# Performance work log

Measured on AMD Instinct MI355X. Metric: run time of the kernel, lower is better.

The kernel has to match this reference:

```python
import jax, jax.numpy as jnp
import numpy as np

B, T, D = 2, 2048, 1024
NH, DH = 16, 64  # inner = NH*DH = D
SCALE_INIT = 0.02


def setup_inputs() -> dict:
    key = jax.random.key(0)
    kx, kq, kk, kv, ko = jax.random.split(key, 5)
    return {
        "x": jax.random.normal(kx, (B, T, D), dtype=jnp.float32),
        "Wq": jax.random.normal(kq, (D, NH * DH), dtype=jnp.float32) * SCALE_INIT,
        "Wk": jax.random.normal(kk, (D, NH * DH), dtype=jnp.float32) * SCALE_INIT,
        "Wv": jax.random.normal(kv, (D, NH * DH), dtype=jnp.float32) * SCALE_INIT,
        "Wo": jax.random.normal(ko, (NH * DH, D), dtype=jnp.float32) * SCALE_INIT,
    }


def reference(x, Wq, Wk, Wv, Wo):
    # x: (B, T, D)
    b, t, _ = x.shape

    def split_heads(h):
        # (B, T, NH*DH) -> (B, NH, T, DH)
        return h.reshape(b, t, NH, DH).transpose(0, 2, 1, 3)

    q = split_heads(x @ Wq)
    k = split_heads(x @ Wk)
    v = split_heads(x @ Wv)

    scale = jnp.asarray(1.0 / np.sqrt(DH), dtype=x.dtype)
    # The per-chunk loop in the original is mathematically equivalent to
    # full causal attention: each query row attends to keys with k_pos <= q_pos.
    scores = jnp.einsum("bhqd,bhkd->bhqk", q, k) * scale  # (B, NH, T, T)
    causal_mask = jnp.arange(t)[None, :] > jnp.arange(t)[:, None]  # k_pos > q_pos
    scores = jnp.where(causal_mask, -jnp.inf, scores)
    attn = jax.nn.softmax(scores, axis=-1)
    attn = jnp.nan_to_num(attn)  # matches torch.nan_to_num (no fully-masked rows in causal case)
    o = jnp.einsum("bhqk,bhkd->bhqd", attn, v)  # (B, NH, T, DH)
    o = o.transpose(0, 2, 1, 3).reshape(b, t, NH * DH)  # merge heads
    return o @ Wo  # (B, T, D)
```

## Files before the change

### kernel.cpp

```cpp
#include <hip/hip_runtime.h>
#include <hip/hip_bf16.h>
#include <string.h>

#define Bsz 2
#define Tsz 2048
#define Dsz 1024
#define NHsz 16
#define Msz (Bsz*Tsz)

typedef unsigned short bfu;
typedef __attribute__((ext_vector_type(8))) short short8;
typedef __attribute__((ext_vector_type(4))) short short4v;
typedef __attribute__((ext_vector_type(4))) float floatx4;

__device__ __forceinline__ bfu f2bf(float f) {
  unsigned int u = __builtin_bit_cast(unsigned int, f);
  u += 0x7fffu + ((u >> 16) & 1u);
  return (bfu)(u >> 16);
}

__device__ __forceinline__ short4v pack4bf(float a, float b, float c_, float d) {
  __hip_bfloat162 h01 = __float22bfloat162_rn(make_float2(a, b));
  __hip_bfloat162 h23 = __float22bfloat162_rn(make_float2(c_, d));
  uint2 uu;
  memcpy(&uu.x, &h01, 4);
  memcpy(&uu.y, &h23, 4);
  return __builtin_bit_cast(short4v, uu);
}

__device__ __forceinline__ short8 pack8bf(float4 a, float4 b) {
  __hip_bfloat162 h0 = __float22bfloat162_rn(make_float2(a.x, a.y));
  __hip_bfloat162 h1 = __float22bfloat162_rn(make_float2(a.z, a.w));
  __hip_bfloat162 h2 = __float22bfloat162_rn(make_float2(b.x, b.y));
  __hip_bfloat162 h3 = __float22bfloat162_rn(make_float2(b.z, b.w));
  uint4 u;
  memcpy(&u.x, &h0, 4); memcpy(&u.y, &h1, 4);
  memcpy(&u.z, &h2, 4); memcpy(&u.w, &h3, 4);
  return __builtin_bit_cast(short8, u);
}

__device__ __forceinline__ void async16(const void* g, void* l) {
  void* gnc = (void*)g;
  __builtin_amdgcn_global_load_lds((__attribute__((address_space(1))) void*)gnc,
                                   (__attribute__((address_space(3))) void*)l,
                                   16, 0, 0);
}

__global__ __launch_bounds__(256) void transpose_w(const float* __restrict__ W0, const float* __restrict__ W1,
                                                   const float* __restrict__ W2, const float* __restrict__ W3,
                                                   bfu* __restrict__ wt) {
  __shared__ float tile[32][33];
  const float* W = blockIdx.z == 0 ? W0 : blockIdx.z == 1 ? W1 : blockIdx.z == 2 ? W2 : W3;
  const float s = (blockIdx.z == 0) ? 0.18033688011112042f : 1.0f;
  bfu* WT = wt + (size_t)blockIdx.z * Dsz * Dsz;
  int tx = threadIdx.x, ty = threadIdx.y;
  int kb = blockIdx.y * 32, nb = blockIdx.x * 32;
#pragma unroll
  for (int i = 0; i < 4; ++i)
    tile[ty + i*8][tx] = W[(size_t)(kb + ty + i*8) * Dsz + nb + tx];
  __syncthreads();
#pragma unroll
  for (int i = 0; i < 4; ++i)
    WT[(size_t)(nb + ty + i*8) * Dsz + kb + tx] = f2bf(tile[tx][ty + i*8] * s);
}

template <bool F32OUT, bool AF32, int NT>
__global__ __launch_bounds__(256) void gemm128(const void* __restrict__ Ain, const bfu* __restrict__ Bt0,
                                               void* __restrict__ C0, int K, int N,
                                               size_t strideB, size_t strideC) {
  constexpr int NJ = NT / 32;
  const int tid = threadIdx.x, wave = tid >> 6, lane = tid & 63;
  const int g = lane >> 4, c = lane & 15;
  const int m0 = blockIdx.y * 128, n0 = blockIdx.x * NT;
  const bfu* Bt = Bt0 + strideB * blockIdx.z;
  __shared__ bfu smem[4096 + NT * 32];
  bfu* As = smem;
  bfu* Bs = smem + 4096;
  floatx4 acc[4][NJ] = {};
  const int srow = lane >> 2, scol = (lane & 3) * 8;
  const bfu* gB = Bt + (size_t)(n0 + srow) * K + scol;
  const int wm = (wave >> 1) * 64, wn = (wave & 1) * (NT / 2);

  short8 areg[2];
  if (AF32) {
#pragma unroll
    for (int cc = 0; cc < 2; ++cc) {
      const float* pa = (const float*)Ain +
          (size_t)(m0 + (wave*2 + cc)*16 + srow) * K + scol;
      areg[cc] = pack8bf(((const float4*)pa)[0], ((const float4*)pa)[1]);
    }
  }
  const bfu* gA = AF32 ? nullptr : (const bfu*)Ain + (size_t)(m0 + srow) * K + scol;

  for (int k0 = 0; k0 < K; k0 += 32) {
    __syncthreads();
#pragma unroll
    for (int cc = 0; cc < 2; ++cc) {
      const int chunk = wave * 2 + cc;
      if (AF32) *(short8*)&As[chunk * 512 + lane * 8] = areg[cc];
      else      async16(gA + (size_t)chunk * 16 * K + k0, &As[chunk * 512]);
    }
#pragma unroll
    for (int cc = 0; cc < NT/64; ++cc) {
      const int chunk = wave * (NT/64) + cc;
      async16(gB + (size_t)chunk * 16 * K + k0, &Bs[chunk * 512]);
    }
    __syncthreads();
    if (AF32 && k0 + 32 < K) {
#pragma unroll
      for (int cc = 0; cc < 2; ++cc) {
        const float* pa = (const float*)Ain +
            (size_t)(m0 + (wave*2 + cc)*16 + srow) * K + (k0 + 32) + scol;
        areg[cc] = pack8bf(((const float4*)pa)[0], ((const float4*)pa)[1]);
      }
    }
    short8 afr[4], bfr[NJ];
#pragma unroll
    for (int t = 0; t < 4; ++t) afr[t] = *(const short8*)&As[(wm + t*16 + c) * 32 + g * 8];
#pragma unroll
    for (int t = 0; t < NJ; ++t) bfr[t] = *(const short8*)&Bs[(wn + t*16 + c) * 32 + g * 8];
#pragma unroll
    for (int i = 0; i < 4; ++i)
#pragma unroll
      for (int j = 0; j < NJ; ++j)
        acc[i][j] = __builtin_amdgcn_mfma_f32_16x16x32_bf16(afr[i], bfr[j], acc[i][j], 0, 0, 0);
  }

  const bool vtrans = (!F32OUT) && (NT == 128) && (blockIdx.z == 2);
  if (vtrans) {
    bfu* vtp = (bfu*)C0 + (size_t)2 * strideC;
#pragma unroll
    for (int p = 0; p < 2; ++p) {
      __syncthreads();
      if ((wave & 1) == p) {
#pragma unroll
        for (int i = 0; i < 4; ++i)
#pragma unroll
          for (int j = 0; j < NJ; ++j) {
            const int nl = j*16 + c;
            const int mg = ((wm + i*16) >> 3) + (g >> 1);
            const int phys = nl * 128 + ((mg ^ (nl & 15)) << 3) + ((g & 1) << 2);
            *(short4v*)&smem[phys] = pack4bf(acc[i][j][0], acc[i][j][1],
                                             acc[i][j][2], acc[i][j][3]);
          }
      }
      __syncthreads();
      const int h_ = (n0 + p * 64) >> 6;
      bfu* dst = vtp + ((size_t)((m0 >> 11) * 16 + h_) * 64) * Tsz + (m0 & 2047);
#pragma unroll
      for (int s = 0; s < 4; ++s) {
        const int nl = s * 16 + (tid >> 4);
        const int me = (tid & 15) << 3;
        const int phys = nl * 128 + (((me >> 3) ^ (nl & 15)) << 3);
        *(short8*)&dst[(size_t)nl * Tsz + me] = *(const short8*)&smem[phys];
      }
    }
    return;
  }

#pragma unroll
  for (int i = 0; i < 4; ++i) {
#pragma unroll
    for (int j = 0; j < NJ; ++j) {
      const int m = m0 + wm + i*16 + g*4;
      const int n = n0 + wn + j*16 + c;
#pragma unroll
      for (int r = 0; r < 4; ++r) {
        float v = acc[i][j][r];
        if (F32OUT) ((float*)C0)[(size_t)(m + r) * N + n] = v;
        else        ((bfu*)C0)[strideC * blockIdx.z + (size_t)(m + r) * N + n] = f2bf(v);
      }
    }
  }
}

__global__ __launch_bounds__(256, 2) void attn_kernel(const bfu* __restrict__ qkv,
                                                      bfu* __restrict__ obuf) {
  const int tid = threadIdx.x, wave = tid >> 6, lane = tid & 63;
  const int g = (lane >> 4) & 3, c = lane & 15, c7 = c & 7;
  const int bh = blockIdx.y, b = bh >> 4, h = bh & 15;
  const size_t hb = (size_t)b * Tsz * Dsz + h * 64;
  const bfu* Qp = qkv + hb;
  const bfu* Kp = qkv + (size_t)Msz * Dsz + hb;
  const bfu* Vt = qkv + (size_t)2 * Msz * Dsz + (size_t)bh * 64 * Tsz;

  __shared__ bfu Ks[128 * 64];
  __shared__ bfu Vs[64 * 128];
  __shared__ bfu Ps[4][16 * 128];

  const int kst_row = lane >> 3;
  const int kst_off = ((lane & 7) ^ kst_row) << 3;
  const int vst_row = lane >> 4;

  for (int half = 0; half < 2; ++half) {
    const int j = half ? (31 - (int)blockIdx.x) : (int)blockIdx.x;
    const int qw = j * 64 + wave * 16;
    const int ktm = j >> 1;

    short8 bq[2];
#pragma unroll
    for (int kk = 0; kk < 2; ++kk)
      bq[kk] = *(const short8*)(Qp + (size_t)(qw + c) * Dsz + kk * 32 + g * 8);

    floatx4 acc[4] = {};
    float mi = -3.0e38f, li = 0.0f;

    for (int kt = 0; kt <= ktm; ++kt) {
      __syncthreads();
#pragma unroll
      for (int cc = 0; cc < 4; ++cc) {
        const int ch = wave * 4 + cc;
        async16(Kp + (size_t)(kt * 128 + ch * 8 + kst_row) * Dsz + kst_off, &Ks[ch * 512]);
        const int drow = ch * 4 + vst_row;
        async16(Vt + (size_t)drow * Tsz + kt * 128 + (((lane & 15) ^ (drow & 7)) << 3), &Vs[ch * 512]);
      }
      __syncthreads();

      floatx4 st[8] = {};
#pragma unroll
      for (int kk = 0; kk < 2; ++kk)
#pragma unroll
        for (int mk = 0; mk < 8; ++mk) {
          const short8 kf = *(const short8*)&Ks[(mk * 16 + c) * 64 + (((kk * 4 + g) ^ c7) << 3)];
          st[mk] = __builtin_amdgcn_mfma_f32_16x16x32_bf16(kf, bq[kk], st[mk], 0, 0, 0);
        }

      if (kt == ktm) {
#pragma unroll
        for (int mk = 0; mk < 8; ++mk) {
          const int keyb = kt * 128 + mk * 16 + g * 4;
#pragma unroll
          for (int r = 0; r < 4; ++r)
            if (keyb + r > qw + c) st[mk][r] = -1.0e38f;
        }
      }

      float mloc = -3.0e38f;
#pragma unroll
      for (int mk = 0; mk < 8; ++mk)
#pragma unroll
        for (int r = 0; r < 4; ++r) mloc = fmaxf(mloc, st[mk][r]);
      mloc = fmaxf(mloc, __shfl_xor(mloc, 16));
      mloc = fmaxf(mloc, __shfl_xor(mloc, 32));
      const float mnew = fmaxf(mi, mloc);
      const float alpha = exp2f(mi - mnew);
      mi = mnew;
      float sum = 0.0f;
#pragma unroll
      for (int mk = 0; mk < 8; ++mk) {
        short4v pk;
#pragma unroll
        for (int r = 0; r < 4; ++r) {
          const float p = exp2f(st[mk][r] - mnew);
          sum += p;
          pk[r] = (short)f2bf(p);
        }
        *(short4v*)&Ps[wave][c * 128 + (((mk * 2 + (g >> 1)) ^ c7) << 3) + ((g & 1) << 2)] = pk;
      }
      sum += __shfl_xor(sum, 16);
      sum += __shfl_xor(sum, 32);
      li = li * alpha + sum;

      float al[4];
#pragma unroll
      for (int r = 0; r < 4; ++r) al[r] = __shfl(alpha, (lane & 48) | (g * 4 + r));
#pragma unroll
      for (int nd = 0; nd < 4; ++nd)
#pragma unroll
        for (int r = 0; r < 4; ++r) acc[nd][r] *= al[r];

#pragma unroll
      for (int kc = 0; kc < 4; ++kc) {
        const int sl = ((kc * 4 + g) ^ c7) << 3;
        const short8 pf = *(const short8*)&Ps[wave][c * 128 + sl];
#pragma unroll
        for (int nd = 0; nd < 4; ++nd) {
          const short8 vf = *(const short8*)&Vs[(nd * 16 + c) * 128 + sl];
          acc[nd] = __builtin_amdgcn_mfma_f32_16x16x32_bf16(pf, vf, acc[nd], 0, 0, 0);
        }
      }
    }

    float inv[4];
#pragma unroll
    for (int r = 0; r < 4; ++r) inv[r] = 1.0f / __shfl(li, (lane & 48) | (g * 4 + r));
#pragma unroll
    for (int nd = 0; nd < 4; ++nd)
#pragma unroll
      for (int r = 0; r < 4; ++r)
        obuf[(size_t)(b * Tsz + qw + g * 4 + r) * Dsz + h * 64 + nd * 16 + c] =
            f2bf(acc[nd][r] * inv[r]);
  }
}

extern "C" void kernel_launch(void* const* d_in, const int* in_sizes, int n_in,
                              void* d_out, int out_size, void* d_ws, size_t ws_size,
                              hipStream_t stream) {
  const float* x  = (const float*)d_in[0];
  const float* Wq = (const float*)d_in[1];
  const float* Wk = (const float*)d_in[2];
  const float* Wv = (const float*)d_in[3];
  const float* Wo = (const float*)d_in[4];
  float* out = (float*)d_out;

  bfu* wt   = (bfu*)d_ws;
  bfu* qkv  = wt  + (size_t)4 * Dsz * Dsz;
  bfu* obuf = qkv + (size_t)3 * Msz * Dsz;

  transpose_w<<<dim3(32, 32, 4), dim3(32, 8), 0, stream>>>(Wq, Wk, Wv, Wo, wt);
  gemm128<false, true, 128><<<dim3(Dsz / 128, Msz / 128, 3), dim3(256), 0, stream>>>(
      (const void*)x, wt, (void*)qkv, Dsz, Dsz, (size_t)Dsz * Dsz, (size_t)Msz * Dsz);
  attn_kernel<<<dim3(16, Bsz * NHsz), dim3(256), 0, stream>>>(qkv, obuf);
  gemm128<true, false, 64><<<dim3(Dsz / 64, Msz / 128, 1), dim3(256), 0, stream>>>(
      (const void*)obuf, wt + (size_t)3 * Dsz * Dsz, (void*)out, Dsz, Dsz,
      (size_t)0, (size_t)0);
}
```

Before: 202.2 us.

## Co-process paired query tiles with double-buffered K/V and register-resident P

```diff
diff --git a/kernel.cpp b/kernel.cpp
--- a/kernel.cpp
+++ b/kernel.cpp
@@ -178,119 +178,200 @@
                                                       bfu* __restrict__ obuf) {
   const int tid = threadIdx.x, wave = tid >> 6, lane = tid & 63;
   const int g = (lane >> 4) & 3, c = lane & 15, c7 = c & 7;
-  const int bh = blockIdx.y, b = bh >> 4, h = bh & 15;
+
+  const int flat = (int)blockIdx.y * 16 + (int)blockIdx.x;
+  const int bh = (flat & 7) * 4 + ((flat >> 3) >> 4);
+  const int jA = (flat >> 3) & 15, jB = 31 - jA;
+  const int b = bh >> 4, h = bh & 15;
+  const int ktmA = jA >> 1;
+  const int ktm = 15 - ktmA;
+
   const size_t hb = (size_t)b * Tsz * Dsz + h * 64;
   const bfu* Qp = qkv + hb;
   const bfu* Kp = qkv + (size_t)Msz * Dsz + hb;
   const bfu* Vt = qkv + (size_t)2 * Msz * Dsz + (size_t)bh * 64 * Tsz;
 
-  __shared__ bfu Ks[128 * 64];
-  __shared__ bfu Vs[64 * 128];
-  __shared__ bfu Ps[4][16 * 128];
+  __shared__ bfu Ks[2][128 * 64];
+  __shared__ bfu Vs[2][64 * 128];
+
+  const int qwA = jA * 64 + wave * 16, qwB = jB * 64 + wave * 16;
+
+  short8 bqA[2], bqB[2];
+#pragma unroll
+  for (int kk = 0; kk < 2; ++kk) {
+    bqA[kk] = *(const short8*)(Qp + (size_t)(qwA + c) * Dsz + kk * 32 + g * 8);
+    bqB[kk] = *(const short8*)(Qp + (size_t)(qwB + c) * Dsz + kk * 32 + g * 8);
+  }
 
   const int kst_row = lane >> 3;
   const int kst_off = ((lane & 7) ^ kst_row) << 3;
   const int vst_row = lane >> 4;
-
-  for (int half = 0; half < 2; ++half) {
-    const int j = half ? (31 - (int)blockIdx.x) : (int)blockIdx.x;
-    const int qw = j * 64 + wave * 16;
-    const int ktm = j >> 1;
-
-    short8 bq[2];
-#pragma unroll
-    for (int kk = 0; kk < 2; ++kk)
-      bq[kk] = *(const short8*)(Qp + (size_t)(qw + c) * Dsz + kk * 32 + g * 8);
-
-    floatx4 acc[4] = {};
-    float mi = -3.0e38f, li = 0.0f;
-
-    for (int kt = 0; kt <= ktm; ++kt) {
-      __syncthreads();
+  const bfu* kpp[4]; const bfu* vpp[4];
+#pragma unroll
+  for (int cc = 0; cc < 4; ++cc) {
+    const int ch = wave * 4 + cc;
+    kpp[cc] = Kp + (size_t)(ch * 8 + kst_row) * Dsz + kst_off;
+    const int drow = ch * 4 + vst_row;
+    vpp[cc] = Vt + (size_t)drow * Tsz + (((lane & 15) ^ (drow & 15)) << 3);
+  }
+
+  floatx4 accA[4] = {}, accB[4] = {};
+  float miA = -3.0e38f, liA = 0.0f, miB = -3.0e38f, liB = 0.0f;
+
+  const floatx4 z4 = {0.0f, 0.0f, 0.0f, 0.0f};
+
+  auto smax = [&](floatx4* st, float& mi, float& li, floatx4* acc,
+                  short4v* pa, int qw, int diag, int ktt) {
+    if (diag) {
+#pragma unroll
+      for (int mk = 0; mk < 8; ++mk) {
+        const int keyb = ktt * 128 + mk * 16 + g * 4;
+#pragma unroll
+        for (int r = 0; r < 4; ++r)
+          if (keyb + r > qw + c) st[mk][r] = -1.0e38f;
+      }
+    }
+    float mloc = -3.0e38f;
+#pragma unroll
+    for (int mk = 0; mk < 8; ++mk)
+      mloc = fmaxf(mloc, fmaxf(fmaxf(st[mk][0], st[mk][1]),
+                               fmaxf(st[mk][2], st[mk][3])));
+    mloc = fmaxf(mloc, __shfl_xor(mloc, 16));
+    mloc = fmaxf(mloc, __shfl_xor(mloc, 32));
+    const float mcand = fmaxf(mi, mloc);
+    const bool resc = !__all(mcand - mi <= 8.0f);
+    const float mnew = resc ? mcand : mi;
+    float sum = 0.0f;
+#pragma unroll
+    for (int mk = 0; mk < 8; ++mk) {
+      const float p0 = exp2f(st[mk][0] - mnew);
+      const float p1 = exp2f(st[mk][1] - mnew);
+      const float p2 = exp2f(st[mk][2] - mnew);
+      const float p3 = exp2f(st[mk][3] - mnew);
+      sum += (p0 + p1) + (p2 + p3);
+      pa[mk] = pack4bf(p0, p1, p2, p3);
+    }
+    sum += __shfl_xor(sum, 16);
+    sum += __shfl_xor(sum, 32);
+    if (resc) {
+      const float alpha = exp2f(mi - mnew);
+      li = li * alpha + sum;
+      mi = mnew;
+      float al[4];
+#pragma unroll
+      for (int r = 0; r < 4; ++r) al[r] = __shfl(alpha, (lane & 48) | (g * 4 + r));
+#pragma unroll
+      for (int nd = 0; nd < 4; ++nd)
+#pragma unroll
+        for (int r = 0; r < 4; ++r) acc[nd][r] *= al[r];
+    } else {
+      li += sum;
+    }
+  };
+
+#pragma unroll
+  for (int cc = 0; cc < 4; ++cc) {
+    const int ch = wave * 4 + cc;
+    async16(kpp[cc], &Ks[0][ch * 512]);
+    async16(vpp[cc], &Vs[0][ch * 512]);
+    kpp[cc] += (size_t)128 * Dsz;
+    vpp[cc] += 128;
+  }
+
+  for (int kt = 0; kt <= ktm; ++kt) {
+    const int cur = kt & 1;
+    if (kt < ktm) {
 #pragma unroll
       for (int cc = 0; cc < 4; ++cc) {
         const int ch = wave * 4 + cc;
-        async16(Kp + (size_t)(kt * 128 + ch * 8 + kst_row) * Dsz + kst_off, &Ks[ch * 512]);
-        const int drow = ch * 4 + vst_row;
-        async16(Vt + (size_t)drow * Tsz + kt * 128 + (((lane & 15) ^ (drow & 7)) << 3), &Vs[ch * 512]);
-      }
-      __syncthreads();
-
-      floatx4 st[8] = {};
+        async16(kpp[cc], &Ks[cur ^ 1][ch * 512]);
+        async16(vpp[cc], &Vs[cur ^ 1][ch * 512]);
+        kpp[cc] += (size_t)128 * Dsz;
+        vpp[cc] += 128;
+      }
+      asm volatile("s_waitcnt vmcnt(8)" ::: "memory");
+    } else {
+      asm volatile("s_waitcnt vmcnt(0)" ::: "memory");
+    }
+    __builtin_amdgcn_s_barrier();
+    asm volatile("" ::: "memory");
+
+    const bfu* KsC = &Ks[cur][0];
+    const bfu* VsC = &Vs[cur][0];
+    const bool doA = (kt <= ktmA);
+
+    floatx4 stA[8], stB[8];
+    __builtin_amdgcn_s_setprio(1);
+    if (doA) {
 #pragma unroll
       for (int kk = 0; kk < 2; ++kk)
 #pragma unroll
         for (int mk = 0; mk < 8; ++mk) {
-          const short8 kf = *(const short8*)&Ks[(mk * 16 + c) * 64 + (((kk * 4 + g) ^ c7) << 3)];
-          st[mk] = __builtin_amdgcn_mfma_f32_16x16x32_bf16(kf, bq[kk], st[mk], 0, 0, 0);
+          const short8 kf = *(const short8*)&KsC[(mk * 16 + c) * 64 + (((kk * 4 + g) ^ c7) << 3)];
+          if (kk == 0) {
+            stA[mk] = __builtin_amdgcn_mfma_f32_16x16x32_bf16(kf, bqA[0], z4, 0, 0, 0);
+            stB[mk] = __builtin_amdgcn_mfma_f32_16x16x32_bf16(kf, bqB[0], z4, 0, 0, 0);
+          } else {
+            stA[mk] = __builtin_amdgcn_mfma_f32_16x16x32_bf16(kf, bqA[1], stA[mk], 0, 0, 0);
+            stB[mk] = __builtin_amdgcn_mfma_f32_16x16x32_bf16(kf, bqB[1], stB[mk], 0, 0, 0);
+          }
         }
-
-      if (kt == ktm) {
+    } else {
+#pragma unroll
+      for (int kk = 0; kk < 2; ++kk)
 #pragma unroll
         for (int mk = 0; mk < 8; ++mk) {
-          const int keyb = kt * 128 + mk * 16 + g * 4;
-#pragma unroll
-          for (int r = 0; r < 4; ++r)
-            if (keyb + r > qw + c) st[mk][r] = -1.0e38f;
+          const short8 kf = *(const short8*)&KsC[(mk * 16 + c) * 64 + (((kk * 4 + g) ^ c7) << 3)];
+          stB[mk] = __builtin_amdgcn_mfma_f32_16x16x32_bf16(kf, bqB[kk],
+                                                            kk ? stB[mk] : z4, 0, 0, 0);
         }
-      }
-
-      float mloc = -3.0e38f;
+    }
+    __builtin_amdgcn_s_setprio(0);
+
+    short4v paA[8], paB[8];
+    if (doA) smax(stA, miA, liA, accA, paA, qwA, kt == ktmA, kt);
+    smax(stB, miB, liB, accB, paB, qwB, kt == ktm, kt);
+
+    __builtin_amdgcn_s_setprio(1);
+    if (doA) {
 #pragma unroll
       for (int mk = 0; mk < 8; ++mk)
 #pragma unroll
-        for (int r = 0; r < 4; ++r) mloc = fmaxf(mloc, st[mk][r]);
-      mloc = fmaxf(mloc, __shfl_xor(mloc, 16));
-      mloc = fmaxf(mloc, __shfl_xor(mloc, 32));
-      const float mnew = fmaxf(mi, mloc);
-      const float alpha = exp2f(mi - mnew);
-      mi = mnew;
-      float sum = 0.0f;
-#pragma unroll
-      for (int mk = 0; mk < 8; ++mk) {
-        short4v pk;
-#pragma unroll
-        for (int r = 0; r < 4; ++r) {
-          const float p = exp2f(st[mk][r] - mnew);
-          sum += p;
-          pk[r] = (short)f2bf(p);
+        for (int nd = 0; nd < 4; ++nd) {
+          const short4v vf = *(const short4v*)&VsC[(nd * 16 + c) * 128 +
+              ((((mk << 1) + (g >> 1)) ^ c) << 3) + ((g & 1) << 2)];
+          accA[nd] = __builtin_amdgcn_mfma_f32_16x16x16bf16_1k(paA[mk], vf, accA[nd], 0, 0, 0);
+          accB[nd] = __builtin_amdgcn_mfma_f32_16x16x16bf16_1k(paB[mk], vf, accB[nd], 0, 0, 0);
         }
-        *(short4v*)&Ps[wave][c * 128 + (((mk * 2 + (g >> 1)) ^ c7) << 3) + ((g & 1) << 2)] = pk;
-      }
-      sum += __shfl_xor(sum, 16);
-      sum += __shfl_xor(sum, 32);
-      li = li * alpha + sum;
-
-      float al[4];
-#pragma unroll
-      for (int r = 0; r < 4; ++r) al[r] = __shfl(alpha, (lane & 48) | (g * 4 + r));
+    } else {
+#pragma unroll
+      for (int mk = 0; mk < 8; ++mk)
+#pragma unroll
+        for (int nd = 0; nd < 4; ++nd) {
+          const short4v vf = *(const short4v*)&VsC[(nd * 16 + c) * 128 +
+              ((((mk << 1) + (g >> 1)) ^ c) << 3) + ((g & 1) << 2)];
+          accB[nd] = __builtin_amdgcn_mfma_f32_16x16x16bf16_1k(paB[mk], vf, accB[nd], 0, 0, 0);
+        }
+    }
+    __builtin_amdgcn_s_setprio(0);
+
+    asm volatile("" ::: "memory");
+    __builtin_amdgcn_s_barrier();
+    asm volatile("" ::: "memory");
+  }
+
+  auto epi = [&](floatx4* acc, float li, int qw) {
+#pragma unroll
+    for (int r = 0; r < 4; ++r) {
+      const float inv = 1.0f / __shfl(li, (lane & 48) | (g * 4 + r));
 #pragma unroll
       for (int nd = 0; nd < 4; ++nd)
-#pragma unroll
-        for (int r = 0; r < 4; ++r) acc[nd][r] *= al[r];
-
-#pragma unroll
-      for (int kc = 0; kc < 4; ++kc) {
-        const int sl = ((kc * 4 + g) ^ c7) << 3;
-        const short8 pf = *(const short8*)&Ps[wave][c * 128 + sl];
-#pragma unroll
-        for (int nd = 0; nd < 4; ++nd) {
-          const short8 vf = *(const short8*)&Vs[(nd * 16 + c) * 128 + sl];
-          acc[nd] = __builtin_amdgcn_mfma_f32_16x16x32_bf16(pf, vf, acc[nd], 0, 0, 0);
-        }
-      }
-    }
-
-    float inv[4];
-#pragma unroll
-    for (int r = 0; r < 4; ++r) inv[r] = 1.0f / __shfl(li, (lane & 48) | (g * 4 + r));
-#pragma unroll
-    for (int nd = 0; nd < 4; ++nd)
-#pragma unroll
-      for (int r = 0; r < 4; ++r)
         obuf[(size_t)(b * Tsz + qw + g * 4 + r) * Dsz + h * 64 + nd * 16 + c] =
-            f2bf(acc[nd][r] * inv[r]);
-  }
+            f2bf(acc[nd][r] * inv);
+    }
+  };
+  epi(accA, liA, qwA);
+  epi(accB, liB, qwB);
 }
 
 extern "C" void kernel_launch(void* const* d_in, const int* in_sizes, int n_in,
```

Result: slower. 208.0 us (+2.9%).

## Restructure causal attention with double-buffered 64-key tiles, register P, lazy rescale

Applied to the files above, without the earlier changes.

```diff
diff --git a/kernel.cpp b/kernel.cpp
--- a/kernel.cpp
+++ b/kernel.cpp
@@ -17,6 +17,14 @@
   unsigned int u = __builtin_bit_cast(unsigned int, f);
   u += 0x7fffu + ((u >> 16) & 1u);
   return (bfu)(u >> 16);
+}
+
+__device__ __forceinline__ float fexp2(float x) {
+#if __has_builtin(__builtin_amdgcn_exp2f)
+  return __builtin_amdgcn_exp2f(x);
+#else
+  return exp2f(x);
+#endif
 }
 
 __device__ __forceinline__ short4v pack4bf(float a, float b, float c_, float d) {
@@ -174,93 +182,129 @@
   }
 }
 
-__global__ __launch_bounds__(256, 2) void attn_kernel(const bfu* __restrict__ qkv,
+__global__ __launch_bounds__(256, 4) void attn_kernel(const bfu* __restrict__ qkv,
                                                       bfu* __restrict__ obuf) {
   const int tid = threadIdx.x, wave = tid >> 6, lane = tid & 63;
   const int g = (lane >> 4) & 3, c = lane & 15, c7 = c & 7;
-  const int bh = blockIdx.y, b = bh >> 4, h = bh & 15;
-  const size_t hb = (size_t)b * Tsz * Dsz + h * 64;
-  const bfu* Qp = qkv + hb;
-  const bfu* Kp = qkv + (size_t)Msz * Dsz + hb;
+
+  const int flat = (int)blockIdx.y * 32 + (int)blockIdx.x;
+  const int xcd = flat & 7, idx = flat >> 3;
+  const int s = idx >> 5, t = idx & 31;
+  const int tt = (s & 2) ? ((t + 16) & 31) : t;
+  const int j  = (s & 1) ? (31 - tt) : tt;
+  const int bh = xcd * 4 + s;
+  const int b = bh >> 4, h = bh & 15;
+
+  const size_t hbq = (size_t)b * Tsz * Dsz + h * 64;
+  const bfu* Qp = qkv + hbq;
+  const bfu* Kp = qkv + (size_t)Msz * Dsz + hbq;
   const bfu* Vt = qkv + (size_t)2 * Msz * Dsz + (size_t)bh * 64 * Tsz;
 
-  __shared__ bfu Ks[128 * 64];
-  __shared__ bfu Vs[64 * 128];
-  __shared__ bfu Ps[4][16 * 128];
-
-  const int kst_row = lane >> 3;
-  const int kst_off = ((lane & 7) ^ kst_row) << 3;
-  const int vst_row = lane >> 4;
-
-  for (int half = 0; half < 2; ++half) {
-    const int j = half ? (31 - (int)blockIdx.x) : (int)blockIdx.x;
-    const int qw = j * 64 + wave * 16;
-    const int ktm = j >> 1;
-
-    short8 bq[2];
-#pragma unroll
-    for (int kk = 0; kk < 2; ++kk)
-      bq[kk] = *(const short8*)(Qp + (size_t)(qw + c) * Dsz + kk * 32 + g * 8);
-
-    floatx4 acc[4] = {};
-    float mi = -3.0e38f, li = 0.0f;
-
-    for (int kt = 0; kt <= ktm; ++kt) {
-      __syncthreads();
-#pragma unroll
-      for (int cc = 0; cc < 4; ++cc) {
-        const int ch = wave * 4 + cc;
-        async16(Kp + (size_t)(kt * 128 + ch * 8 + kst_row) * Dsz + kst_off, &Ks[ch * 512]);
-        const int drow = ch * 4 + vst_row;
-        async16(Vt + (size_t)drow * Tsz + kt * 128 + (((lane & 15) ^ (drow & 7)) << 3), &Vs[ch * 512]);
-      }
-      __syncthreads();
-
-      floatx4 st[8] = {};
-#pragma unroll
-      for (int kk = 0; kk < 2; ++kk)
-#pragma unroll
-        for (int mk = 0; mk < 8; ++mk) {
-          const short8 kf = *(const short8*)&Ks[(mk * 16 + c) * 64 + (((kk * 4 + g) ^ c7) << 3)];
-          st[mk] = __builtin_amdgcn_mfma_f32_16x16x32_bf16(kf, bq[kk], st[mk], 0, 0, 0);
-        }
-
-      if (kt == ktm) {
-#pragma unroll
-        for (int mk = 0; mk < 8; ++mk) {
-          const int keyb = kt * 128 + mk * 16 + g * 4;
-#pragma unroll
-          for (int r = 0; r < 4; ++r)
-            if (keyb + r > qw + c) st[mk][r] = -1.0e38f;
-        }
-      }
-
-      float mloc = -3.0e38f;
-#pragma unroll
-      for (int mk = 0; mk < 8; ++mk)
-#pragma unroll
-        for (int r = 0; r < 4; ++r) mloc = fmaxf(mloc, st[mk][r]);
-      mloc = fmaxf(mloc, __shfl_xor(mloc, 16));
-      mloc = fmaxf(mloc, __shfl_xor(mloc, 32));
-      const float mnew = fmaxf(mi, mloc);
-      const float alpha = exp2f(mi - mnew);
+  __shared__ bfu Ks[2][64 * 64];
+  __shared__ bfu Vs[2][64 * 64];
+
+  const int qw = j * 64 + wave * 16;
+
+  short8 bq[2];
+#pragma unroll
+  for (int kk = 0; kk < 2; ++kk)
+    bq[kk] = *(const short8*)(Qp + (size_t)(qw + c) * Dsz + kk * 32 + g * 8);
+
+  const int srow8 = lane >> 3;
+  const int soff = ((lane & 7) ^ srow8) << 3;
+  const bfu* kpp[2]; const bfu* vpp[2];
+#pragma unroll
+  for (int cc = 0; cc < 2; ++cc) {
+    const int ch = wave * 2 + cc;
+    kpp[cc] = Kp + (size_t)(ch * 8 + srow8) * Dsz + soff;
+    vpp[cc] = Vt + (size_t)(ch * 8 + srow8) * Tsz + soff;
+  }
+
+  floatx4 acc[4] = {};
+  float mi = -3.0e38f, li = 0.0f;
+  const floatx4 z4 = {0.0f, 0.0f, 0.0f, 0.0f};
+
+#pragma unroll
+  for (int cc = 0; cc < 2; ++cc) {
+    const int ch = wave * 2 + cc;
+    async16(kpp[cc], &Ks[0][ch * 512]);
+    async16(vpp[cc], &Vs[0][ch * 512]);
+    kpp[cc] += (size_t)64 * Dsz;
+    vpp[cc] += 64;
+  }
+
+  for (int kt = 0; kt <= j; ++kt) {
+    const int cur = kt & 1;
+    if (kt < j) {
+#pragma unroll
+      for (int cc = 0; cc < 2; ++cc) {
+        const int ch = wave * 2 + cc;
+        async16(kpp[cc], &Ks[cur ^ 1][ch * 512]);
+        async16(vpp[cc], &Vs[cur ^ 1][ch * 512]);
+        kpp[cc] += (size_t)64 * Dsz;
+        vpp[cc] += 64;
+      }
+      asm volatile("s_waitcnt vmcnt(4)" ::: "memory");
+    } else {
+      asm volatile("s_waitcnt vmcnt(0)" ::: "memory");
+    }
+    __builtin_amdgcn_s_barrier();
+    asm volatile("" ::: "memory");
+
+    const bfu* KsC = &Ks[cur][0];
+    const bfu* VsC = &Vs[cur][0];
+
+    floatx4 st[4];
+    __builtin_amdgcn_s_setprio(1);
+#pragma unroll
+    for (int mk = 0; mk < 4; ++mk) {
+      const short8 kf = *(const short8*)&KsC[(mk * 16 + c) * 64 + ((g ^ c7) << 3)];
+      st[mk] = __builtin_amdgcn_mfma_f32_16x16x32_bf16(kf, bq[0], z4, 0, 0, 0);
+    }
+#pragma unroll
+    for (int mk = 0; mk < 4; ++mk) {
+      const short8 kf = *(const short8*)&KsC[(mk * 16 + c) * 64 + (((4 + g) ^ c7) << 3)];
+      st[mk] = __builtin_amdgcn_mfma_f32_16x16x32_bf16(kf, bq[1], st[mk], 0, 0, 0);
+    }
+    __builtin_amdgcn_s_setprio(0);
+
+    if (kt == j) {
+#pragma unroll
+      for (int mk = 0; mk < 4; ++mk) {
+        const int keyb = kt * 64 + mk * 16 + g * 4;
+#pragma unroll
+        for (int r = 0; r < 4; ++r)
+          if (keyb + r > qw + c) st[mk][r] = -1.0e38f;
+      }
+    }
+
+    float mloc = -3.0e38f;
+#pragma unroll
+    for (int mk = 0; mk < 4; ++mk)
+      mloc = fmaxf(mloc, fmaxf(fmaxf(st[mk][0], st[mk][1]),
+                               fmaxf(st[mk][2], st[mk][3])));
+    mloc = fmaxf(mloc, __shfl_xor(mloc, 16));
+    mloc = fmaxf(mloc, __shfl_xor(mloc, 32));
+    const float mcand = fmaxf(mi, mloc);
+    const bool resc = !__all(mcand - mi <= 8.0f);
+    const float mnew = resc ? mcand : mi;
+    float sum = 0.0f;
+    short4v pa[4];
+#pragma unroll
+    for (int mk = 0; mk < 4; ++mk) {
+      const float p0 = fexp2(st[mk][0] - mnew);
+      const float p1 = fexp2(st[mk][1] - mnew);
+      const float p2 = fexp2(st[mk][2] - mnew);
+      const float p3 = fexp2(st[mk][3] - mnew);
+      sum += (p0 + p1) + (p2 + p3);
+      pa[mk] = pack4bf(p0, p1, p2, p3);
+    }
+    sum += __shfl_xor(sum, 16);
+    sum += __shfl_xor(sum, 32);
+    if (resc) {
+      const float alpha = fexp2(mi - mnew);
+      li = li * alpha + sum;
       mi = mnew;
-      float sum = 0.0f;
-#pragma unroll
-      for (int mk = 0; mk < 8; ++mk) {
-        short4v pk;
-#pragma unroll
-        for (int r = 0; r < 4; ++r) {
-          const float p = exp2f(st[mk][r] - mnew);
-          sum += p;
-          pk[r] = (short)f2bf(p);
-        }
-        *(short4v*)&Ps[wave][c * 128 + (((mk * 2 + (g >> 1)) ^ c7) << 3) + ((g & 1) << 2)] = pk;
-      }
-      sum += __shfl_xor(sum, 16);
-      sum += __shfl_xor(sum, 32);
-      li = li * alpha + sum;
-
       float al[4];
 #pragma unroll
       for (int r = 0; r < 4; ++r) al[r] = __shfl(alpha, (lane & 48) | (g * 4 + r));
@@ -268,28 +312,33 @@
       for (int nd = 0; nd < 4; ++nd)
 #pragma unroll
         for (int r = 0; r < 4; ++r) acc[nd][r] *= al[r];
-
-#pragma unroll
-      for (int kc = 0; kc < 4; ++kc) {
-        const int sl = ((kc * 4 + g) ^ c7) << 3;
-        const short8 pf = *(const short8*)&Ps[wave][c * 128 + sl];
-#pragma unroll
-        for (int nd = 0; nd < 4; ++nd) {
-          const short8 vf = *(const short8*)&Vs[(nd * 16 + c) * 128 + sl];
-          acc[nd] = __builtin_amdgcn_mfma_f32_16x16x32_bf16(pf, vf, acc[nd], 0, 0, 0);
-        }
-      }
-    }
-
-    float inv[4];
-#pragma unroll
-    for (int r = 0; r < 4; ++r) inv[r] = 1.0f / __shfl(li, (lane & 48) | (g * 4 + r));
+    } else {
+      li += sum;
+    }
+
+    __builtin_amdgcn_s_setprio(1);
+#pragma unroll
+    for (int mk = 0; mk < 4; ++mk)
+#pragma unroll
+      for (int nd = 0; nd < 4; ++nd) {
+        const short4v vf = *(const short4v*)&VsC[(nd * 16 + c) * 64 +
+            ((((mk << 1) + (g >> 1)) ^ c7) << 3) + ((g & 1) << 2)];
+        acc[nd] = __builtin_amdgcn_mfma_f32_16x16x16bf16_1k(pa[mk], vf, acc[nd], 0, 0, 0);
+      }
+    __builtin_amdgcn_s_setprio(0);
+
+    asm volatile("" ::: "memory");
+    __builtin_amdgcn_s_barrier();
+    asm volatile("" ::: "memory");
+  }
+
+#pragma unroll
+  for (int r = 0; r < 4; ++r) {
+    const float inv = 1.0f / __shfl(li, (lane & 48) | (g * 4 + r));
 #pragma unroll
     for (int nd = 0; nd < 4; ++nd)
-#pragma unroll
-      for (int r = 0; r < 4; ++r)
-        obuf[(size_t)(b * Tsz + qw + g * 4 + r) * Dsz + h * 64 + nd * 16 + c] =
-            f2bf(acc[nd][r] * inv[r]);
+      obuf[(size_t)(b * Tsz + qw + g * 4 + r) * Dsz + h * 64 + nd * 16 + c] =
+          f2bf(acc[nd][r] * inv);
   }
 }
 
@@ -310,7 +359,7 @@
   transpose_w<<<dim3(32, 32, 4), dim3(32, 8), 0, stream>>>(Wq, Wk, Wv, Wo, wt);
   gemm128<false, true, 128><<<dim3(Dsz / 128, Msz / 128, 3), dim3(256), 0, stream>>>(
       (const void*)x, wt, (void*)qkv, Dsz, Dsz, (size_t)Dsz * Dsz, (size_t)Msz * Dsz);
-  attn_kernel<<<dim3(16, Bsz * NHsz), dim3(256), 0, stream>>>(qkv, obuf);
+  attn_kernel<<<dim3(32, 32), dim3(256), 0, stream>>>(qkv, obuf);
   gemm128<true, false, 64><<<dim3(Dsz / 64, Msz / 128, 1), dim3(256), 0, stream>>>(
       (const void*)obuf, wt + (size_t)3 * Dsz * Dsz, (void*)out, Dsz, Dsz,
       (size_t)0, (size_t)0);
```

After: 199.3 us. No clear change (-1.4%).
